# Optimization experiments

Hardware: AMD Instinct MI355X
Metric: run time of the kernel (lower is better)

## Reference

```python
import jax, jax.numpy as jnp
import numpy as np

N = 100000   # nodes
E = 1600000  # edges
F = 128      # input node features
H = 128      # hidden channels
G = 512      # graphs in batch
EPS = 1e-5   # BatchNorm eps


def setup_inputs() -> dict:
    key = jax.random.key(0)
    ks = jax.random.split(key, 24)
    x = jax.random.normal(ks[0], (N, F), jnp.float32)
    edge_index = jax.random.randint(ks[1], (2, E), 0, N)
    batch = jnp.sort(jax.random.randint(ks[2], (N,), 0, G))

    def lin_w(k, i, o):
        return jax.random.normal(k, (i, o), jnp.float32) / np.sqrt(i)

    inp = {
        "x": x, "edge_index": edge_index, "batch": batch,
        "W1": lin_w(ks[3], F, H), "b1": jnp.zeros((H,), jnp.float32),
        "g1": jnp.ones((H,), jnp.float32), "be1": jnp.zeros((H,), jnp.float32),
        "m1": 0.1 * jax.random.normal(ks[4], (H,), jnp.float32),
        "v1": jax.random.uniform(ks[5], (H,), jnp.float32) + 0.5,
        "W2": lin_w(ks[6], H, H), "b2": jnp.zeros((H,), jnp.float32),
        "g2": jnp.ones((H,), jnp.float32), "be2": jnp.zeros((H,), jnp.float32),
        "m2": 0.1 * jax.random.normal(ks[7], (H,), jnp.float32),
        "v2": jax.random.uniform(ks[8], (H,), jnp.float32) + 0.5,
        "W3": lin_w(ks[9], H, H), "b3": jnp.zeros((H,), jnp.float32),
        "g3": jnp.ones((H,), jnp.float32), "be3": jnp.zeros((H,), jnp.float32),
        "m3": 0.1 * jax.random.normal(ks[10], (H,), jnp.float32),
        "v3": jax.random.uniform(ks[11], (H,), jnp.float32) + 0.5,
        "Wl": lin_w(ks[12], H, 1), "bl": jnp.zeros((1,), jnp.float32),
    }
    return inp


def _gcn_norm(edge_index):
    # add self-loops, then symmetric normalization deg^-1/2 A_hat deg^-1/2
    loops = jnp.arange(N)
    src = jnp.concatenate([edge_index[0], loops])
    dst = jnp.concatenate([edge_index[1], loops])
    deg = jax.ops.segment_sum(jnp.ones_like(src, jnp.float32), dst, num_segments=N)
    dinv = jax.lax.rsqrt(jnp.maximum(deg, 1.0))
    norm = dinv[src] * dinv[dst]  # [E+N]
    return src, dst, norm


def _gcn_conv(x, W, b, src, dst, norm):
    h = x @ W                                    # [N,H] dense GEMM first (PyG order)
    msg = h[src] * norm[:, None]                 # gather + scale, [E+N,H]
    agg = jax.ops.segment_sum(msg, dst, num_segments=N)  # scatter-add
    return agg + b


def _bn_relu(x, g, be, m, v):
    # inference BatchNorm1d (running stats) + ReLU
    return jax.nn.relu((x - m) * jax.lax.rsqrt(v + EPS) * g + be)


def reference(x, edge_index, batch,
              W1, b1, g1, be1, m1, v1,
              W2, b2, g2, be2, m2, v2,
              W3, b3, g3, be3, m3, v3,
              Wl, bl):
    src, dst, norm = _gcn_norm(edge_index)
    h = _bn_relu(_gcn_conv(x, W1, b1, src, dst, norm), g1, be1, m1, v1)
    h = _bn_relu(_gcn_conv(h, W2, b2, src, dst, norm), g2, be2, m2, v2)
    h = _bn_relu(_gcn_conv(h, W3, b3, src, dst, norm), g3, be3, m3, v3)
    # global mean pool over graphs
    sums = jax.ops.segment_sum(h, batch, num_segments=G)           # [G,H]
    cnt = jax.ops.segment_sum(jnp.ones((N,), jnp.float32), batch, num_segments=G)
    pooled = sums / jnp.maximum(cnt, 1.0)[:, None]
    # dropout is identity at inference; final linear
    return pooled @ Wl + bl  # [G,1]
```

## Files before the change

kernel.cpp:

```cpp
#include <hip/hip_runtime.h>
#include <hip/hip_bf16.h>

#define NN 100000
#define NE 1600000
#define HD 128
#define NG 512
#define BN_EPS 1e-5f

#define GEMM_BLOCKS 1563
#define NODES_PER_BLK 16
#define GATH_BLOCKS (NN / NODES_PER_BLK)

#define BIN_SHIFT 8
#define NBIN 391
#define TILE 4096
#define NBLK_BIN 391

typedef __attribute__((ext_vector_type(8))) short short8;
typedef __attribute__((ext_vector_type(4))) float floatx4;

__device__ __forceinline__ ushort f2bf(float f) {
    union { float f; uint u; } v; v.f = f;
    uint r = (v.u + 0x7FFF + ((v.u >> 16) & 1)) >> 16;
    return (ushort)r;
}
__device__ __forceinline__ float bflo(uint u) { union { uint u; float f; } v; v.u = u << 16; return v.f; }
__device__ __forceinline__ float bfhi(uint u) { union { uint u; float f; } v; v.u = u & 0xFFFF0000u; return v.f; }

__global__ void k_prep_all(const float* __restrict__ W1, const float* __restrict__ W2,
                           const float* __restrict__ W3,
                           ushort* __restrict__ Wt1, ushort* __restrict__ Wt2,
                           ushort* __restrict__ Wt3,
                           const float* __restrict__ b1, const float* __restrict__ g1,
                           const float* __restrict__ be1, const float* __restrict__ m1,
                           const float* __restrict__ v1,
                           const float* __restrict__ b2, const float* __restrict__ g2,
                           const float* __restrict__ be2, const float* __restrict__ m2,
                           const float* __restrict__ v2,
                           const float* __restrict__ b3, const float* __restrict__ g3,
                           const float* __restrict__ be3, const float* __restrict__ m3,
                           const float* __restrict__ v3,
                           float* scale1, float* shift1, float* scale2, float* shift2,
                           float* scale3, float* shift3,
                           const int* __restrict__ bat, float* __restrict__ invcnt,
                           float* __restrict__ out2d) {
    int blk = blockIdx.x, tid = threadIdx.x;
    if (blk < 192) {
        int w = blk >> 6;
        int i = (blk & 63) * 256 + tid;
        const float* W = (w == 0) ? W1 : (w == 1) ? W2 : W3;
        ushort* Wt = (w == 0) ? Wt1 : (w == 1) ? Wt2 : Wt3;
        int k = i >> 7, n = i & 127;
        Wt[n * 128 + k] = f2bf(W[i]);
    } else if (blk < 195) {
        if (tid < 128) {
            int l = blk - 192;
            const float *b, *g, *be, *m, *v;
            float *sc, *sh;
            if (l == 0)      { b = b1; g = g1; be = be1; m = m1; v = v1; sc = scale1; sh = shift1; }
            else if (l == 1) { b = b2; g = g2; be = be2; m = m2; v = v2; sc = scale2; sh = shift2; }
            else             { b = b3; g = g3; be = be3; m = m3; v = v3; sc = scale3; sh = shift3; }
            float s = g[tid] * rsqrtf(v[tid] + BN_EPS);
            sc[tid] = s;
            sh[tid] = (b[tid] - m[tid]) * s + be[tid];
        }
    } else {
        int g = (blk - 195) * 256 + tid;
        if (g < NG) {
            int lo = 0, hi = NN;
            while (lo < hi) { int mid = (lo + hi) >> 1; if (bat[mid] < g) lo = mid + 1; else hi = mid; }
            int lo2 = lo, hi2 = NN;
            while (lo2 < hi2) { int mid = (lo2 + hi2) >> 1; if (bat[mid] < g + 1) lo2 = mid + 1; else hi2 = mid; }
            int cnt = lo2 - lo;
            invcnt[g] = 1.f / fmaxf((float)cnt, 1.f);
#pragma unroll
            for (int i = 0; i < 8; ++i) out2d[g * 8 + i] = 0.f;
        }
    }
}

__launch_bounds__(256)
__global__ void k_fused1(const float* __restrict__ x, const ushort* __restrict__ Wt,
                         ushort* __restrict__ hs,
                         const int* __restrict__ dst, int* __restrict__ L) {
    __shared__ int lh[NBIN];
    const int tid = threadIdx.x;
    if (blockIdx.x >= GEMM_BLOCKS) {
        int blk = blockIdx.x - GEMM_BLOCKS;
        for (int i = tid; i < NBIN; i += 256) lh[i] = 0;
        __syncthreads();
        long base = (long)blk * TILE;
#pragma unroll 4
        for (int i = 0; i < TILE / 256; ++i) {
            long e = base + i * 256 + tid;
            if (e < NE) atomicAdd(&lh[dst[e] >> BIN_SHIFT], 1);
        }
        __syncthreads();
        for (int i = tid; i < NBIN; i += 256) L[i * NBLK_BIN + blk] = lh[i];
        return;
    }
    const int wave = tid >> 6, lane = tid & 63;
    const int m = lane & 15, kg = lane >> 4;
    const long row0 = (long)blockIdx.x * 64 + wave * 16;

    long arow = row0 + m;
    long arc = arow < NN ? arow : (NN - 1);
    const float* xf = x + arc * 128;
    short8 a[4];
#pragma unroll
    for (int s = 0; s < 4; ++s) {
        float4 f0 = *(const float4*)(xf + s * 32 + kg * 8);
        float4 f1 = *(const float4*)(xf + s * 32 + kg * 8 + 4);
        short8 t;
        t[0] = (short)f2bf(f0.x); t[1] = (short)f2bf(f0.y);
        t[2] = (short)f2bf(f0.z); t[3] = (short)f2bf(f0.w);
        t[4] = (short)f2bf(f1.x); t[5] = (short)f2bf(f1.y);
        t[6] = (short)f2bf(f1.z); t[7] = (short)f2bf(f1.w);
        a[s] = t;
    }

    floatx4 acc[8];
#pragma unroll
    for (int ct = 0; ct < 8; ++ct) acc[ct] = (floatx4){0.f, 0.f, 0.f, 0.f};

#pragma unroll
    for (int s = 0; s < 4; ++s) {
#pragma unroll
        for (int ct = 0; ct < 8; ++ct) {
            short8 b = *(const short8*)(Wt + (ct * 16 + m) * 128 + s * 32 + kg * 8);
            acc[ct] = __builtin_amdgcn_mfma_f32_16x16x32_bf16(a[s], b, acc[ct], 0, 0, 0);
        }
    }

#pragma unroll
    for (int r = 0; r < 4; ++r) {
        long orow = row0 + kg * 4 + r;
        if (orow < NN) {
#pragma unroll
            for (int ct = 0; ct < 8; ++ct)
                hs[orow * 128 + ct * 16 + m] = f2bf(acc[ct][r]);
        }
    }
}

__global__ void k_scanA(int* __restrict__ L, int* __restrict__ binTot) {
    __shared__ int s[512];
    int b = blockIdx.x, t = threadIdx.x;
    int v = (t < NBLK_BIN) ? L[b * NBLK_BIN + t] : 0;
    s[t] = v;
    __syncthreads();
    for (int o = 1; o < 512; o <<= 1) {
        int x = (t >= o) ? s[t - o] : 0;
        __syncthreads();
        s[t] += x;
        __syncthreads();
    }
    if (t < NBLK_BIN) L[b * NBLK_BIN + t] = s[t] - v;
    if (t == 511) binTot[b] = s[511];
}

__global__ void k_scanB(const int* __restrict__ binTot, int* __restrict__ bin_ebase,
                        int* __restrict__ rs) {
    __shared__ int s[512];
    int t = threadIdx.x;
    int v = (t < NBIN) ? binTot[t] : 0;
    s[t] = v;
    __syncthreads();
    for (int o = 1; o < 512; o <<= 1) {
        int x = (t >= o) ? s[t - o] : 0;
        __syncthreads();
        s[t] += x;
        __syncthreads();
    }
    if (t < NBIN) bin_ebase[t] = s[t] - v;
    if (t == 0) { bin_ebase[NBIN] = NE; rs[NN] = NE; }
}

__launch_bounds__(256)
__global__ void k_binscatter(const int* __restrict__ src, const int* __restrict__ dst,
                             const int* __restrict__ L, const int* __restrict__ bin_ebase,
                             uint* __restrict__ bpack) {
    __shared__ int off[NBIN];
    int t = threadIdx.x, blk = blockIdx.x;
    for (int i = t; i < NBIN; i += 256) off[i] = L[i * NBLK_BIN + blk] + bin_ebase[i];
    __syncthreads();
    long base = (long)blk * TILE;
#pragma unroll 4
    for (int i = 0; i < TILE / 256; ++i) {
        long e = base + i * 256 + t;
        if (e < NE) {
            int d = dst[e];
            int p = atomicAdd(&off[d >> BIN_SHIFT], 1);
            bpack[p] = (uint)src[e] | ((uint)(d & 255) << 24);
        }
    }
}

__launch_bounds__(256)
__global__ void k_bincsr(const uint* __restrict__ bpack, const int* __restrict__ bin_ebase,
                         int* __restrict__ rs, float* __restrict__ dinv,
                         int* __restrict__ csr) {
    __shared__ int cnt[256];
    __shared__ int sc[256];
    __shared__ int run[256];
    int t = threadIdx.x, b = blockIdx.x;
    int e0 = bin_ebase[b], e1 = bin_ebase[b + 1];
    cnt[t] = 0;
    __syncthreads();
    for (int e = e0 + t; e < e1; e += 256) atomicAdd(&cnt[bpack[e] >> 24], 1);
    __syncthreads();
    int c = cnt[t];
    sc[t] = c;
    __syncthreads();
    for (int o = 1; o < 256; o <<= 1) {
        int x = (t >= o) ? sc[t - o] : 0;
        __syncthreads();
        sc[t] += x;
        __syncthreads();
    }
    int excl = sc[t] - c;
    int node = (b << BIN_SHIFT) + t;
    if (node < NN) {
        rs[node] = e0 + excl;
        dinv[node] = rsqrtf((float)(c + 1));
    }
    run[t] = e0 + excl;
    __syncthreads();
    for (int e = e0 + t; e < e1; e += 256) {
        uint u = bpack[e];
        int p = atomicAdd(&run[u >> 24], 1);
        csr[p] = (int)(u & 0xFFFFFFu);
    }
}

#define WT_STRIDE 136
__launch_bounds__(256)
__global__ void k_gemm_l23(const ushort* __restrict__ xb, const ushort* __restrict__ Wt,
                           const float* __restrict__ dinv, ushort* __restrict__ hs) {
    __shared__ ushort sWt[128 * WT_STRIDE];
    const int tid = threadIdx.x;
    for (int i = tid; i < 2048; i += 256) {
        int row = i >> 4, seg = i & 15;
        *(uint4*)&sWt[row * WT_STRIDE + seg * 8] = *(const uint4*)(Wt + row * 128 + seg * 8);
    }
    __syncthreads();

    const int wave = tid >> 6, lane = tid & 63;
    const int m = lane & 15, kg = lane >> 4;
    const long row0 = (long)blockIdx.x * 64 + wave * 16;

    long arow = row0 + m;
    long arc = arow < NN ? arow : (NN - 1);
    short8 a[4];
#pragma unroll
    for (int s = 0; s < 4; ++s)
        a[s] = *(const short8*)(xb + arc * 128 + s * 32 + kg * 8);

    floatx4 acc[8];
#pragma unroll
    for (int ct = 0; ct < 8; ++ct) acc[ct] = (floatx4){0.f, 0.f, 0.f, 0.f};

#pragma unroll
    for (int s = 0; s < 4; ++s) {
#pragma unroll
        for (int ct = 0; ct < 8; ++ct) {
            short8 b = *(const short8*)&sWt[(ct * 16 + m) * WT_STRIDE + s * 32 + kg * 8];
            acc[ct] = __builtin_amdgcn_mfma_f32_16x16x32_bf16(a[s], b, acc[ct], 0, 0, 0);
        }
    }

#pragma unroll
    for (int r = 0; r < 4; ++r) {
        long orow = row0 + kg * 4 + r;
        if (orow < NN) {
            float dd = dinv[orow];
#pragma unroll
            for (int ct = 0; ct < 8; ++ct)
                hs[orow * 128 + ct * 16 + m] = f2bf(acc[ct][r] * dd);
        }
    }
}

template <bool SCALE_SRC, bool POOL>
__launch_bounds__(256)
__global__ void k_gather_w(const ushort* __restrict__ hs, const int* __restrict__ rs,
                           const int* __restrict__ csr, const float* __restrict__ dinv,
                           const float* __restrict__ scale, const float* __restrict__ shift,
                           ushort* __restrict__ xout,
                           const int* __restrict__ bat, const float* __restrict__ invcnt,
                           const float* __restrict__ Wl, float* __restrict__ out2d) {
    __shared__ int nextn;
    const int tid = threadIdx.x;
    if (tid == 0) nextn = 0;
    __syncthreads();
    const int lane = tid & 63;
    const int sub = lane >> 4;
    const int c0 = (lane & 15) * 8;
    const int base = blockIdx.x * NODES_PER_BLK;

    for (int it = 0; it <= NODES_PER_BLK; ++it) {
        int myn = 0;
        if (lane == 0) myn = atomicAdd(&nextn, 1);
        myn = __shfl(myn, 0);
        if (myn >= NODES_PER_BLK) break;
        const int d = base + myn;

        const int e0 = rs[d], e1 = rs[d + 1];
        const float dd = dinv[d];

        float a0 = 0.f, a1 = 0.f, a2 = 0.f, a3 = 0.f,
              a4 = 0.f, a5 = 0.f, a6 = 0.f, a7 = 0.f;

        if (sub == 0) {
            uint4 sv = *(const uint4*)(hs + (long)d * 128 + c0);
            float w = SCALE_SRC ? dd : 1.0f;
            a0 = w * bflo(sv.x); a1 = w * bfhi(sv.x);
            a2 = w * bflo(sv.y); a3 = w * bfhi(sv.y);
            a4 = w * bflo(sv.z); a5 = w * bfhi(sv.z);
            a6 = w * bflo(sv.w); a7 = w * bfhi(sv.w);
        }

        int j = e0 + sub;
        int s0 = 0, s1 = 0, s2 = 0, s3 = 0;
        bool have = (j + 12 < e1);
        if (have) { s0 = csr[j]; s1 = csr[j + 4]; s2 = csr[j + 8]; s3 = csr[j + 12]; }
        while (have) {
            int jn = j + 16;
            bool nxt = (jn + 12 < e1);
            int n0 = 0, n1 = 0, n2 = 0, n3 = 0;
            if (nxt) { n0 = csr[jn]; n1 = csr[jn + 4]; n2 = csr[jn + 8]; n3 = csr[jn + 12]; }
            float w0 = 1.f, w1 = 1.f, w2 = 1.f, w3 = 1.f;
            if (SCALE_SRC) { w0 = dinv[s0]; w1 = dinv[s1]; w2 = dinv[s2]; w3 = dinv[s3]; }
            uint4 v0 = *(const uint4*)(hs + (long)s0 * 128 + c0);
            uint4 v1 = *(const uint4*)(hs + (long)s1 * 128 + c0);
            uint4 v2 = *(const uint4*)(hs + (long)s2 * 128 + c0);
            uint4 v3 = *(const uint4*)(hs + (long)s3 * 128 + c0);
            a0 += w0 * bflo(v0.x) + w1 * bflo(v1.x) + w2 * bflo(v2.x) + w3 * bflo(v3.x);
            a1 += w0 * bfhi(v0.x) + w1 * bfhi(v1.x) + w2 * bfhi(v2.x) + w3 * bfhi(v3.x);
            a2 += w0 * bflo(v0.y) + w1 * bflo(v1.y) + w2 * bflo(v2.y) + w3 * bflo(v3.y);
            a3 += w0 * bfhi(v0.y) + w1 * bfhi(v1.y) + w2 * bfhi(v2.y) + w3 * bfhi(v3.y);
            a4 += w0 * bflo(v0.z) + w1 * bflo(v1.z) + w2 * bflo(v2.z) + w3 * bflo(v3.z);
            a5 += w0 * bfhi(v0.z) + w1 * bfhi(v1.z) + w2 * bfhi(v2.z) + w3 * bfhi(v3.z);
            a6 += w0 * bflo(v0.w) + w1 * bflo(v1.w) + w2 * bflo(v2.w) + w3 * bflo(v3.w);
            a7 += w0 * bfhi(v0.w) + w1 * bfhi(v1.w) + w2 * bfhi(v2.w) + w3 * bfhi(v3.w);
            j = jn; s0 = n0; s1 = n1; s2 = n2; s3 = n3; have = nxt;
        }
        if (j < e1) {
            bool b1 = (j + 4) < e1, b2 = (j + 8) < e1;
            int t0 = csr[j];
            int t1 = b1 ? csr[j + 4] : t0;
            int t2 = b2 ? csr[j + 8] : t0;
            float w0 = SCALE_SRC ? dinv[t0] : 1.f;
            float w1 = b1 ? (SCALE_SRC ? dinv[t1] : 1.f) : 0.f;
            float w2 = b2 ? (SCALE_SRC ? dinv[t2] : 1.f) : 0.f;
            uint4 v0 = *(const uint4*)(hs + (long)t0 * 128 + c0);
            uint4 v1 = *(const uint4*)(hs + (long)t1 * 128 + c0);
            uint4 v2 = *(const uint4*)(hs + (long)t2 * 128 + c0);
            a0 += w0 * bflo(v0.x) + w1 * bflo(v1.x) + w2 * bflo(v2.x);
            a1 += w0 * bfhi(v0.x) + w1 * bfhi(v1.x) + w2 * bfhi(v2.x);
            a2 += w0 * bflo(v0.y) + w1 * bflo(v1.y) + w2 * bflo(v2.y);
            a3 += w0 * bfhi(v0.y) + w1 * bfhi(v1.y) + w2 * bfhi(v2.y);
            a4 += w0 * bflo(v0.z) + w1 * bflo(v1.z) + w2 * bflo(v2.z);
            a5 += w0 * bfhi(v0.z) + w1 * bfhi(v1.z) + w2 * bfhi(v2.z);
            a6 += w0 * bflo(v0.w) + w1 * bflo(v1.w) + w2 * bflo(v2.w);
            a7 += w0 * bfhi(v0.w) + w1 * bfhi(v1.w) + w2 * bfhi(v2.w);
        }

        a0 += __shfl_xor(a0, 16); a1 += __shfl_xor(a1, 16);
        a2 += __shfl_xor(a2, 16); a3 += __shfl_xor(a3, 16);
        a4 += __shfl_xor(a4, 16); a5 += __shfl_xor(a5, 16);
        a6 += __shfl_xor(a6, 16); a7 += __shfl_xor(a7, 16);
        a0 += __shfl_xor(a0, 32); a1 += __shfl_xor(a1, 32);
        a2 += __shfl_xor(a2, 32); a3 += __shfl_xor(a3, 32);
        a4 += __shfl_xor(a4, 32); a5 += __shfl_xor(a5, 32);
        a6 += __shfl_xor(a6, 32); a7 += __shfl_xor(a7, 32);

        float pd = 0.f;
        if (sub == 0) {
            float4 sca = *(const float4*)(scale + c0);
            float4 scb = *(const float4*)(scale + c0 + 4);
            float4 sha = *(const float4*)(shift + c0);
            float4 shb = *(const float4*)(shift + c0 + 4);
            float r0 = fmaxf(dd * a0 * sca.x + sha.x, 0.f);
            float r1 = fmaxf(dd * a1 * sca.y + sha.y, 0.f);
            float r2 = fmaxf(dd * a2 * sca.z + sha.z, 0.f);
            float r3 = fmaxf(dd * a3 * sca.w + sha.w, 0.f);
            float r4 = fmaxf(dd * a4 * scb.x + shb.x, 0.f);
            float r5 = fmaxf(dd * a5 * scb.y + shb.y, 0.f);
            float r6 = fmaxf(dd * a6 * scb.z + shb.z, 0.f);
            float r7 = fmaxf(dd * a7 * scb.w + shb.w, 0.f);
            if constexpr (POOL) {
                float4 wa = *(const float4*)(Wl + c0);
                float4 wb = *(const float4*)(Wl + c0 + 4);
                pd = r0 * wa.x + r1 * wa.y + r2 * wa.z + r3 * wa.w +
                     r4 * wb.x + r5 * wb.y + r6 * wb.z + r7 * wb.w;
            } else {
                uint4 o;
                o.x = (uint)f2bf(r0) | ((uint)f2bf(r1) << 16);
                o.y = (uint)f2bf(r2) | ((uint)f2bf(r3) << 16);
                o.z = (uint)f2bf(r4) | ((uint)f2bf(r5) << 16);
                o.w = (uint)f2bf(r6) | ((uint)f2bf(r7) << 16);
                *(uint4*)(xout + (long)d * 128 + c0) = o;
            }
        }
        if constexpr (POOL) {
            pd += __shfl_xor(pd, 1);
            pd += __shfl_xor(pd, 2);
            pd += __shfl_xor(pd, 4);
            pd += __shfl_xor(pd, 8);
            if (lane == 0) {
                int g = bat[d];
                atomicAdd(&out2d[g * 8 + (d & 7)], pd * invcnt[g]);
            }
        }
    }
}

__global__ void k_final(const float* __restrict__ out2d, const float* __restrict__ bl,
                        float* __restrict__ out) {
    int g = blockIdx.x * 256 + threadIdx.x;
    if (g >= NG) return;
    float s = bl[0];
#pragma unroll
    for (int i = 0; i < 8; ++i) s += out2d[g * 8 + i];
    out[g] = s;
}

extern "C" void kernel_launch(void* const* d_in, const int* in_sizes, int n_in,
                              void* d_out, int out_size, void* d_ws, size_t ws_size,
                              hipStream_t stream) {
    const float* x   = (const float*)d_in[0];
    const int*   ei  = (const int*)d_in[1];
    const int*   bat = (const int*)d_in[2];
    const float* W1  = (const float*)d_in[3];
    const float* b1  = (const float*)d_in[4];
    const float* g1  = (const float*)d_in[5];
    const float* be1 = (const float*)d_in[6];
    const float* m1  = (const float*)d_in[7];
    const float* v1  = (const float*)d_in[8];
    const float* W2  = (const float*)d_in[9];
    const float* b2  = (const float*)d_in[10];
    const float* g2  = (const float*)d_in[11];
    const float* be2 = (const float*)d_in[12];
    const float* m2  = (const float*)d_in[13];
    const float* v2  = (const float*)d_in[14];
    const float* W3  = (const float*)d_in[15];
    const float* b3  = (const float*)d_in[16];
    const float* g3  = (const float*)d_in[17];
    const float* be3 = (const float*)d_in[18];
    const float* m3  = (const float*)d_in[19];
    const float* v3  = (const float*)d_in[20];
    const float* Wl  = (const float*)d_in[21];
    const float* bl  = (const float*)d_in[22];
    float* out = (float*)d_out;

    const int* srcp = ei;
    const int* dstp = ei + NE;

    char* ws = (char*)d_ws;
    size_t off = 0;
    auto alloc = [&](size_t bytes) { char* p = ws + off; off += (bytes + 255) & ~255ULL; return p; };
    float*  dinv     = (float*) alloc(NN * 4);
    int*    rs       = (int*)   alloc((NN + 1) * 4);
    int*    L        = (int*)   alloc((size_t)NBIN * NBLK_BIN * 4);
    int*    binTot   = (int*)   alloc((NBIN + 1) * 4);
    int*    bin_ebase= (int*)   alloc((NBIN + 1) * 4);
    uint*   bpack    = (uint*)  alloc((size_t)NE * 4);
    int*    csr      = (int*)   alloc((size_t)NE * 4);
    float*  scale1 = (float*) alloc(HD * 4);
    float*  shift1 = (float*) alloc(HD * 4);
    float*  scale2 = (float*) alloc(HD * 4);
    float*  shift2 = (float*) alloc(HD * 4);
    float*  scale3 = (float*) alloc(HD * 4);
    float*  shift3 = (float*) alloc(HD * 4);
    float*  invcnt = (float*) alloc(NG * 4);
    float*  out2d  = (float*) alloc(NG * 8 * 4);
    ushort* Wt1    = (ushort*)alloc(128 * 128 * 2);
    ushort* Wt2    = (ushort*)alloc(128 * 128 * 2);
    ushort* Wt3    = (ushort*)alloc(128 * 128 * 2);
    ushort* hs     = (ushort*)alloc((size_t)NN * HD * 2);
    ushort* xbuf   = (ushort*)alloc((size_t)NN * HD * 2);

    k_prep_all<<<197, 256, 0, stream>>>(W1, W2, W3, Wt1, Wt2, Wt3,
                                        b1, g1, be1, m1, v1, b2, g2, be2, m2, v2,
                                        b3, g3, be3, m3, v3,
                                        scale1, shift1, scale2, shift2, scale3, shift3,
                                        bat, invcnt, out2d);

    k_fused1<<<GEMM_BLOCKS + NBLK_BIN, 256, 0, stream>>>(x, Wt1, hs, dstp, L);

    k_scanA<<<NBIN, 512, 0, stream>>>(L, binTot);
    k_scanB<<<1, 512, 0, stream>>>(binTot, bin_ebase, rs);
    k_binscatter<<<NBLK_BIN, 256, 0, stream>>>(srcp, dstp, L, bin_ebase, bpack);
    k_bincsr<<<NBIN, 256, 0, stream>>>(bpack, bin_ebase, rs, dinv, csr);

    k_gather_w<true, false><<<GATH_BLOCKS, 256, 0, stream>>>(
        hs, rs, csr, dinv, scale1, shift1, xbuf, nullptr, nullptr, nullptr, nullptr);
    k_gemm_l23<<<GEMM_BLOCKS, 256, 0, stream>>>(xbuf, Wt2, dinv, hs);
    k_gather_w<false, false><<<GATH_BLOCKS, 256, 0, stream>>>(
        hs, rs, csr, dinv, scale2, shift2, xbuf, nullptr, nullptr, nullptr, nullptr);
    k_gemm_l23<<<GEMM_BLOCKS, 256, 0, stream>>>(xbuf, Wt3, dinv, hs);
    k_gather_w<false, true><<<GATH_BLOCKS, 256, 0, stream>>>(
        hs, rs, csr, dinv, scale3, shift3, nullptr, bat, invcnt, Wl, out2d);

    k_final<<<2, 256, 0, stream>>>(out2d, bl, out);
}
```

Measured before the change: 460.4 us.

## Fuse neighbor gather with next-layer GEMM via shared-memory staging

Gather+BN+ReLU for 64 nodes per block now writes bf16 activations into an LDS tile, and the block then multiplies that tile by the next layer's weights with MFMA. This drops the intermediate activation round-trip through global memory and two kernel launches. The new GEMM reads the weight operand directly from global memory instead of an LDS copy. Moving from 16 to 64 nodes per block gives fewer blocks, which may hurt load balance across the gather.

```diff
diff --git a/kernel.cpp b/kernel.cpp
--- a/kernel.cpp
+++ b/kernel.cpp
@@ -233,62 +233,13 @@
     }
 }
 
-#define WT_STRIDE 136
+template <bool SCALE_SRC>
 __launch_bounds__(256)
-__global__ void k_gemm_l23(const ushort* __restrict__ xb, const ushort* __restrict__ Wt,
-                           const float* __restrict__ dinv, ushort* __restrict__ hs) {
-    __shared__ ushort sWt[128 * WT_STRIDE];
-    const int tid = threadIdx.x;
-    for (int i = tid; i < 2048; i += 256) {
-        int row = i >> 4, seg = i & 15;
-        *(uint4*)&sWt[row * WT_STRIDE + seg * 8] = *(const uint4*)(Wt + row * 128 + seg * 8);
-    }
-    __syncthreads();
-
-    const int wave = tid >> 6, lane = tid & 63;
-    const int m = lane & 15, kg = lane >> 4;
-    const long row0 = (long)blockIdx.x * 64 + wave * 16;
-
-    long arow = row0 + m;
-    long arc = arow < NN ? arow : (NN - 1);
-    short8 a[4];
-#pragma unroll
-    for (int s = 0; s < 4; ++s)
-        a[s] = *(const short8*)(xb + arc * 128 + s * 32 + kg * 8);
-
-    floatx4 acc[8];
-#pragma unroll
-    for (int ct = 0; ct < 8; ++ct) acc[ct] = (floatx4){0.f, 0.f, 0.f, 0.f};
-
-#pragma unroll
-    for (int s = 0; s < 4; ++s) {
-#pragma unroll
-        for (int ct = 0; ct < 8; ++ct) {
-            short8 b = *(const short8*)&sWt[(ct * 16 + m) * WT_STRIDE + s * 32 + kg * 8];
-            acc[ct] = __builtin_amdgcn_mfma_f32_16x16x32_bf16(a[s], b, acc[ct], 0, 0, 0);
-        }
-    }
-
-#pragma unroll
-    for (int r = 0; r < 4; ++r) {
-        long orow = row0 + kg * 4 + r;
-        if (orow < NN) {
-            float dd = dinv[orow];
-#pragma unroll
-            for (int ct = 0; ct < 8; ++ct)
-                hs[orow * 128 + ct * 16 + m] = f2bf(acc[ct][r] * dd);
-        }
-    }
-}
-
-template <bool SCALE_SRC, bool POOL>
-__launch_bounds__(256)
-__global__ void k_gather_w(const ushort* __restrict__ hs, const int* __restrict__ rs,
-                           const int* __restrict__ csr, const float* __restrict__ dinv,
-                           const float* __restrict__ scale, const float* __restrict__ shift,
-                           ushort* __restrict__ xout,
-                           const int* __restrict__ bat, const float* __restrict__ invcnt,
-                           const float* __restrict__ Wl, float* __restrict__ out2d) {
+__global__ void k_gath_gemm(const ushort* __restrict__ hs, const int* __restrict__ rs,
+                            const int* __restrict__ csr, const float* __restrict__ dinv,
+                            const float* __restrict__ scale, const float* __restrict__ shift,
+                            const ushort* __restrict__ Wt, ushort* __restrict__ hout) {
+    __shared__ ushort A[64 * 136];
     __shared__ int nextn;
     const int tid = threadIdx.x;
     if (tid == 0) nextn = 0;
@@ -296,14 +247,18 @@
     const int lane = tid & 63;
     const int sub = lane >> 4;
     const int c0 = (lane & 15) * 8;
-    const int base = blockIdx.x * NODES_PER_BLK;
-
-    for (int it = 0; it <= NODES_PER_BLK; ++it) {
+    const int base = blockIdx.x * 64;
+
+    for (int it = 0; it <= 64; ++it) {
         int myn = 0;
         if (lane == 0) myn = atomicAdd(&nextn, 1);
         myn = __shfl(myn, 0);
-        if (myn >= NODES_PER_BLK) break;
+        if (myn >= 64) break;
         const int d = base + myn;
+        if (d >= NN) {
+            if (sub == 0) { uint4 z = {0u, 0u, 0u, 0u}; *(uint4*)&A[myn * 136 + c0] = z; }
+            continue;
+        }
 
         const int e0 = rs[d], e1 = rs[d + 1];
         const float dd = dinv[d];
@@ -375,6 +330,151 @@
         a4 += __shfl_xor(a4, 32); a5 += __shfl_xor(a5, 32);
         a6 += __shfl_xor(a6, 32); a7 += __shfl_xor(a7, 32);
 
+        if (sub == 0) {
+            float4 sca = *(const float4*)(scale + c0);
+            float4 scb = *(const float4*)(scale + c0 + 4);
+            float4 sha = *(const float4*)(shift + c0);
+            float4 shb = *(const float4*)(shift + c0 + 4);
+            float r0 = fmaxf(dd * a0 * sca.x + sha.x, 0.f);
+            float r1 = fmaxf(dd * a1 * sca.y + sha.y, 0.f);
+            float r2 = fmaxf(dd * a2 * sca.z + sha.z, 0.f);
+            float r3 = fmaxf(dd * a3 * sca.w + sha.w, 0.f);
+            float r4 = fmaxf(dd * a4 * scb.x + shb.x, 0.f);
+            float r5 = fmaxf(dd * a5 * scb.y + shb.y, 0.f);
+            float r6 = fmaxf(dd * a6 * scb.z + shb.z, 0.f);
+            float r7 = fmaxf(dd * a7 * scb.w + shb.w, 0.f);
+            uint4 o;
+            o.x = (uint)f2bf(r0) | ((uint)f2bf(r1) << 16);
+            o.y = (uint)f2bf(r2) | ((uint)f2bf(r3) << 16);
+            o.z = (uint)f2bf(r4) | ((uint)f2bf(r5) << 16);
+            o.w = (uint)f2bf(r6) | ((uint)f2bf(r7) << 16);
+            *(uint4*)&A[myn * 136 + c0] = o;
+        }
+    }
+    __syncthreads();
+
+    const int wave = tid >> 6;
+    const int m = lane & 15, kg = lane >> 4;
+    const long row0 = (long)base + wave * 16;
+
+    short8 a[4];
+#pragma unroll
+    for (int s = 0; s < 4; ++s)
+        a[s] = *(const short8*)&A[(wave * 16 + m) * 136 + s * 32 + kg * 8];
+
+    floatx4 acc[8];
+#pragma unroll
+    for (int ct = 0; ct < 8; ++ct) acc[ct] = (floatx4){0.f, 0.f, 0.f, 0.f};
+
+#pragma unroll
+    for (int s = 0; s < 4; ++s) {
+#pragma unroll
+        for (int ct = 0; ct < 8; ++ct) {
+            short8 b = *(const short8*)(Wt + (ct * 16 + m) * 128 + s * 32 + kg * 8);
+            acc[ct] = __builtin_amdgcn_mfma_f32_16x16x32_bf16(a[s], b, acc[ct], 0, 0, 0);
+        }
+    }
+
+#pragma unroll
+    for (int r = 0; r < 4; ++r) {
+        long orow = row0 + kg * 4 + r;
+        if (orow < NN) {
+            float dd2 = dinv[orow];
+#pragma unroll
+            for (int ct = 0; ct < 8; ++ct)
+                hout[orow * 128 + ct * 16 + m] = f2bf(acc[ct][r] * dd2);
+        }
+    }
+}
+
+__launch_bounds__(256)
+__global__ void k_gather_pool(const ushort* __restrict__ hs, const int* __restrict__ rs,
+                              const int* __restrict__ csr, const float* __restrict__ dinv,
+                              const float* __restrict__ scale, const float* __restrict__ shift,
+                              const int* __restrict__ bat, const float* __restrict__ invcnt,
+                              const float* __restrict__ Wl, float* __restrict__ out2d) {
+    __shared__ int nextn;
+    const int tid = threadIdx.x;
+    if (tid == 0) nextn = 0;
+    __syncthreads();
+    const int lane = tid & 63;
+    const int sub = lane >> 4;
+    const int c0 = (lane & 15) * 8;
+    const int base = blockIdx.x * NODES_PER_BLK;
+
+    for (int it = 0; it <= NODES_PER_BLK; ++it) {
+        int myn = 0;
+        if (lane == 0) myn = atomicAdd(&nextn, 1);
+        myn = __shfl(myn, 0);
+        if (myn >= NODES_PER_BLK) break;
+        const int d = base + myn;
+
+        const int e0 = rs[d], e1 = rs[d + 1];
+        const float dd = dinv[d];
+
+        float a0 = 0.f, a1 = 0.f, a2 = 0.f, a3 = 0.f,
+              a4 = 0.f, a5 = 0.f, a6 = 0.f, a7 = 0.f;
+
+        if (sub == 0) {
+            uint4 sv = *(const uint4*)(hs + (long)d * 128 + c0);
+            a0 = bflo(sv.x); a1 = bfhi(sv.x);
+            a2 = bflo(sv.y); a3 = bfhi(sv.y);
+            a4 = bflo(sv.z); a5 = bfhi(sv.z);
+            a6 = bflo(sv.w); a7 = bfhi(sv.w);
+        }
+
+        int j = e0 + sub;
+        int s0 = 0, s1 = 0, s2 = 0, s3 = 0;
+        bool have = (j + 12 < e1);
+        if (have) { s0 = csr[j]; s1 = csr[j + 4]; s2 = csr[j + 8]; s3 = csr[j + 12]; }
+        while (have) {
+            int jn = j + 16;
+            bool nxt = (jn + 12 < e1);
+            int n0 = 0, n1 = 0, n2 = 0, n3 = 0;
+            if (nxt) { n0 = csr[jn]; n1 = csr[jn + 4]; n2 = csr[jn + 8]; n3 = csr[jn + 12]; }
+            uint4 v0 = *(const uint4*)(hs + (long)s0 * 128 + c0);
+            uint4 v1 = *(const uint4*)(hs + (long)s1 * 128 + c0);
+            uint4 v2 = *(const uint4*)(hs + (long)s2 * 128 + c0);
+            uint4 v3 = *(const uint4*)(hs + (long)s3 * 128 + c0);
+            a0 += bflo(v0.x) + bflo(v1.x) + bflo(v2.x) + bflo(v3.x);
+            a1 += bfhi(v0.x) + bfhi(v1.x) + bfhi(v2.x) + bfhi(v3.x);
+            a2 += bflo(v0.y) + bflo(v1.y) + bflo(v2.y) + bflo(v3.y);
+            a3 += bfhi(v0.y) + bfhi(v1.y) + bfhi(v2.y) + bfhi(v3.y);
+            a4 += bflo(v0.z) + bflo(v1.z) + bflo(v2.z) + bflo(v3.z);
+            a5 += bfhi(v0.z) + bfhi(v1.z) + bfhi(v2.z) + bfhi(v3.z);
+            a6 += bflo(v0.w) + bflo(v1.w) + bflo(v2.w) + bflo(v3.w);
+            a7 += bfhi(v0.w) + bfhi(v1.w) + bfhi(v2.w) + bfhi(v3.w);
+            j = jn; s0 = n0; s1 = n1; s2 = n2; s3 = n3; have = nxt;
+        }
+        if (j < e1) {
+            bool b1 = (j + 4) < e1, b2 = (j + 8) < e1;
+            int t0 = csr[j];
+            int t1 = b1 ? csr[j + 4] : t0;
+            int t2 = b2 ? csr[j + 8] : t0;
+            float w1 = b1 ? 1.f : 0.f;
+            float w2 = b2 ? 1.f : 0.f;
+            uint4 v0 = *(const uint4*)(hs + (long)t0 * 128 + c0);
+            uint4 v1 = *(const uint4*)(hs + (long)t1 * 128 + c0);
+            uint4 v2 = *(const uint4*)(hs + (long)t2 * 128 + c0);
+            a0 += bflo(v0.x) + w1 * bflo(v1.x) + w2 * bflo(v2.x);
+            a1 += bfhi(v0.x) + w1 * bfhi(v1.x) + w2 * bfhi(v2.x);
+            a2 += bflo(v0.y) + w1 * bflo(v1.y) + w2 * bflo(v2.y);
+            a3 += bfhi(v0.y) + w1 * bfhi(v1.y) + w2 * bfhi(v2.y);
+            a4 += bflo(v0.z) + w1 * bflo(v1.z) + w2 * bflo(v2.z);
+            a5 += bfhi(v0.z) + w1 * bfhi(v1.z) + w2 * bfhi(v2.z);
+            a6 += bflo(v0.w) + w1 * bflo(v1.w) + w2 * bflo(v2.w);
+            a7 += bfhi(v0.w) + w1 * bfhi(v1.w) + w2 * bfhi(v2.w);
+        }
+
+        a0 += __shfl_xor(a0, 16); a1 += __shfl_xor(a1, 16);
+        a2 += __shfl_xor(a2, 16); a3 += __shfl_xor(a3, 16);
+        a4 += __shfl_xor(a4, 16); a5 += __shfl_xor(a5, 16);
+        a6 += __shfl_xor(a6, 16); a7 += __shfl_xor(a7, 16);
+        a0 += __shfl_xor(a0, 32); a1 += __shfl_xor(a1, 32);
+        a2 += __shfl_xor(a2, 32); a3 += __shfl_xor(a3, 32);
+        a4 += __shfl_xor(a4, 32); a5 += __shfl_xor(a5, 32);
+        a6 += __shfl_xor(a6, 32); a7 += __shfl_xor(a7, 32);
+
         float pd = 0.f;
         if (sub == 0) {
             float4 sca = *(const float4*)(scale + c0);
@@ -389,29 +489,18 @@
             float r5 = fmaxf(dd * a5 * scb.y + shb.y, 0.f);
             float r6 = fmaxf(dd * a6 * scb.z + shb.z, 0.f);
             float r7 = fmaxf(dd * a7 * scb.w + shb.w, 0.f);
-            if constexpr (POOL) {
-                float4 wa = *(const float4*)(Wl + c0);
-                float4 wb = *(const float4*)(Wl + c0 + 4);
-                pd = r0 * wa.x + r1 * wa.y + r2 * wa.z + r3 * wa.w +
-                     r4 * wb.x + r5 * wb.y + r6 * wb.z + r7 * wb.w;
-            } else {
-                uint4 o;
-                o.x = (uint)f2bf(r0) | ((uint)f2bf(r1) << 16);
-                o.y = (uint)f2bf(r2) | ((uint)f2bf(r3) << 16);
-                o.z = (uint)f2bf(r4) | ((uint)f2bf(r5) << 16);
-                o.w = (uint)f2bf(r6) | ((uint)f2bf(r7) << 16);
-                *(uint4*)(xout + (long)d * 128 + c0) = o;
-            }
-        }
-        if constexpr (POOL) {
-            pd += __shfl_xor(pd, 1);
-            pd += __shfl_xor(pd, 2);
-            pd += __shfl_xor(pd, 4);
-            pd += __shfl_xor(pd, 8);
-            if (lane == 0) {
-                int g = bat[d];
-                atomicAdd(&out2d[g * 8 + (d & 7)], pd * invcnt[g]);
-            }
+            float4 wa = *(const float4*)(Wl + c0);
+            float4 wb = *(const float4*)(Wl + c0 + 4);
+            pd = r0 * wa.x + r1 * wa.y + r2 * wa.z + r3 * wa.w +
+                 r4 * wb.x + r5 * wb.y + r6 * wb.z + r7 * wb.w;
+        }
+        pd += __shfl_xor(pd, 1);
+        pd += __shfl_xor(pd, 2);
+        pd += __shfl_xor(pd, 4);
+        pd += __shfl_xor(pd, 8);
+        if (lane == 0) {
+            int g = bat[d];
+            atomicAdd(&out2d[g * 8 + (d & 7)], pd * invcnt[g]);
         }
     }
 }
@@ -494,14 +583,12 @@
     k_binscatter<<<NBLK_BIN, 256, 0, stream>>>(srcp, dstp, L, bin_ebase, bpack);
     k_bincsr<<<NBIN, 256, 0, stream>>>(bpack, bin_ebase, rs, dinv, csr);
 
-    k_gather_w<true, false><<<GATH_BLOCKS, 256, 0, stream>>>(
-        hs, rs, csr, dinv, scale1, shift1, xbuf, nullptr, nullptr, nullptr, nullptr);
-    k_gemm_l23<<<GEMM_BLOCKS, 256, 0, stream>>>(xbuf, Wt2, dinv, hs);
-    k_gather_w<false, false><<<GATH_BLOCKS, 256, 0, stream>>>(
-        hs, rs, csr, dinv, scale2, shift2, xbuf, nullptr, nullptr, nullptr, nullptr);
-    k_gemm_l23<<<GEMM_BLOCKS, 256, 0, stream>>>(xbuf, Wt3, dinv, hs);
-    k_gather_w<false, true><<<GATH_BLOCKS, 256, 0, stream>>>(
-        hs, rs, csr, dinv, scale3, shift3, nullptr, bat, invcnt, Wl, out2d);
+    k_gath_gemm<true><<<GEMM_BLOCKS, 256, 0, stream>>>(
+        hs, rs, csr, dinv, scale1, shift1, Wt2, xbuf);
+    k_gath_gemm<false><<<GEMM_BLOCKS, 256, 0, stream>>>(
+        xbuf, rs, csr, dinv, scale2, shift2, Wt3, hs);
+    k_gather_pool<<<GATH_BLOCKS, 256, 0, stream>>>(
+        hs, rs, csr, dinv, scale3, shift3, bat, invcnt, Wl, out2d);
 
     k_final<<<2, 256, 0, stream>>>(out2d, bl, out);
 }
```

New measurement: 537.5 us. 1.17x slower.
